# Optimization experiments

Measured on AMD Instinct MI355X. Metric: run time of the kernel, lower is better.

Reference implementation:

```python
import jax, jax.numpy as jnp
import numpy as np

HIDDEN = 2048
NUM_HEADS = 16
NUM_KV_HEADS = 4
HEAD_DIM = HIDDEN // NUM_HEADS  # 128
GROUPS = NUM_HEADS // NUM_KV_HEADS  # 4
ROPE_DIMS = 32
QK_GAIN = 6.0
B, T = 2, 2048


def _rope_cos_sin(T, dtype):
    pos = jnp.arange(T, dtype=jnp.float32)
    inv_freq = 1.0 / (10000.0 ** (jnp.arange(0, ROPE_DIMS, 2, dtype=jnp.float32) / ROPE_DIMS))
    freqs = jnp.outer(pos, inv_freq)                  # [T, ROPE/2]
    freqs = jnp.concatenate([freqs, freqs], axis=-1)  # [T, ROPE]
    return jnp.cos(freqs).astype(dtype), jnp.sin(freqs).astype(dtype)


def _apply_rope(t, cos_f, sin_f):
    # t: [B, H, T, head_dim]; rope on first ROPE_DIMS, pass-through on the rest
    t_rt, t_pass = t[..., :ROPE_DIMS], t[..., ROPE_DIMS:]
    h1, h2 = jnp.split(t_rt, 2, axis=-1)
    rot = jnp.concatenate([-h2, h1], axis=-1)
    return jnp.concatenate([t_rt * cos_f + rot * sin_f, t_pass], axis=-1)


def setup_inputs() -> dict:
    key = jax.random.key(0)
    ks = jax.random.split(key, 5)
    s = 0.02
    return {
        "x": jax.random.normal(ks[0], (B, T, HIDDEN), jnp.float32),
        "Wq": jax.random.normal(ks[1], (HIDDEN, HIDDEN), jnp.float32) * s,
        "Wk": jax.random.normal(ks[2], (HIDDEN, NUM_KV_HEADS * HEAD_DIM), jnp.float32) * s,
        "Wv": jax.random.normal(ks[3], (HIDDEN, NUM_KV_HEADS * HEAD_DIM), jnp.float32) * s,
        "Wo": jax.random.normal(ks[4], (HIDDEN, HIDDEN), jnp.float32) * s,
    }


def reference(x, Wq, Wk, Wv, Wo):
    Bx, Tx, C = x.shape
    q = (x @ Wq).reshape(Bx, Tx, NUM_HEADS, HEAD_DIM).transpose(0, 2, 1, 3)      # [B,H,T,d]
    k = (x @ Wk).reshape(Bx, Tx, NUM_KV_HEADS, HEAD_DIM).transpose(0, 2, 1, 3)   # [B,KV,T,d]
    v = (x @ Wv).reshape(Bx, Tx, NUM_KV_HEADS, HEAD_DIM).transpose(0, 2, 1, 3)   # [B,KV,T,d]

    cos_f, sin_f = _rope_cos_sin(Tx, q.dtype)  # [T, ROPE]
    q = _apply_rope(q, cos_f, sin_f)
    k = _apply_rope(k, cos_f, sin_f)

    # GQA: group query heads per kv head instead of repeat_interleave-ing K/V
    qg = q.reshape(Bx, NUM_KV_HEADS, GROUPS, Tx, HEAD_DIM)
    scale = QK_GAIN / jnp.sqrt(jnp.asarray(HEAD_DIM, q.dtype))
    scores = jnp.einsum('bkgqd,bkld->bkgql', qg * scale, k)  # [B,KV,G,T,T]
    causal = jnp.tril(jnp.ones((Tx, Tx), dtype=bool))
    scores = jnp.where(causal, scores, jnp.asarray(-jnp.inf, scores.dtype))
    probs = jax.nn.softmax(scores, axis=-1)
    out = jnp.einsum('bkgql,bkld->bkgqd', probs, v)          # [B,KV,G,T,d]
    out = out.reshape(Bx, NUM_HEADS, Tx, HEAD_DIM).transpose(0, 2, 1, 3).reshape(Bx, Tx, C)
    return out @ Wo
```

## Files before the change

kernel.cpp:

```cpp
#include <hip/hip_runtime.h>
#include <hip/hip_bf16.h>
#include <cstdint>
#include <cstddef>

typedef unsigned short u16;
typedef short s16x8 __attribute__((ext_vector_type(8)));
typedef float f32x4 __attribute__((ext_vector_type(4)));
typedef float f32x16 __attribute__((ext_vector_type(16)));
typedef u16 u16x4 __attribute__((ext_vector_type(4)));

#define HIDDEN_C 2048
#define TSEQ 2048
#define BATCH 2
#define NHEADS 16
#define NKV 4
#define HDIM 128
#define NQKV 3072
#define BTR 4096
#define QK_SCALE 0.53033008588991f

__device__ __forceinline__ float bf2f(u16 u) {
  union { uint32_t i; float f; } v; v.i = ((uint32_t)u) << 16; return v.f;
}
__device__ __forceinline__ u16 f2bf(float f) {
  union { float f; uint32_t i; } v; v.f = f;
  uint32_t r = v.i + 0x7fffu + ((v.i >> 16) & 1u);
  return (u16)(r >> 16);
}

#define AS1(p) ((__attribute__((address_space(1))) void*)(uintptr_t)(p))
#define AS3(p) ((__attribute__((address_space(3))) void*)(p))

__global__ void convert_x_kernel(const float* __restrict__ x, u16* __restrict__ xb) {
  int i = (blockIdx.x * blockDim.x + threadIdx.x) * 8;
  float4 a = *(const float4*)(x + i);
  float4 b = *(const float4*)(x + i + 4);
  uint4 o;
  o.x = (uint32_t)f2bf(a.x) | ((uint32_t)f2bf(a.y) << 16);
  o.y = (uint32_t)f2bf(a.z) | ((uint32_t)f2bf(a.w) << 16);
  o.z = (uint32_t)f2bf(b.x) | ((uint32_t)f2bf(b.y) << 16);
  o.w = (uint32_t)f2bf(b.z) | ((uint32_t)f2bf(b.w) << 16);
  *(uint4*)(xb + i) = o;
}

__global__ void rope_table_kernel(float2* __restrict__ tab) {
  int idx = blockIdx.x * blockDim.x + threadIdx.x;
  int t = idx >> 4, i = idx & 15;
  float f = powf(10000.f, -(float)i * (1.f / 16.f));
  float ang = (float)t * f;
  tab[idx] = make_float2(cosf(ang), sinf(ang));
}

__global__ void transpose_w_kernel(const float* __restrict__ in, u16* __restrict__ out,
                                   int R, int C) {
  __shared__ float tile[32][33];
  int r0 = blockIdx.y * 32, c0 = blockIdx.x * 32;
  int tx = threadIdx.x, ty = threadIdx.y;
  #pragma unroll
  for (int i = 0; i < 32; i += 8)
    tile[ty + i][tx] = in[(size_t)(r0 + ty + i) * C + c0 + tx];
  __syncthreads();
  #pragma unroll
  for (int i = 0; i < 32; i += 8)
    out[(size_t)(c0 + ty + i) * R + r0 + tx] = f2bf(tile[tx][ty + i]);
}

template <typename OutT>
__global__ __launch_bounds__(256) void gemm_bt_kernel(const u16* __restrict__ A,
                                                      const u16* __restrict__ BT,
                                                      OutT* __restrict__ C,
                                                      int M, int N, int K,
                                                      const float2* __restrict__ tab,
                                                      int mode) {
  __shared__ u16 As[128 * 32];
  __shared__ u16 Bs[128 * 32];
  const int tid = threadIdx.x;
  const int wave = tid >> 6, lane = tid & 63;
  const int lr = lane & 15, lg = lane >> 4;
  const int m0 = blockIdx.y * 128, n0 = blockIdx.x * 128;
  const int wr = wave >> 1, wc = wave & 1;
  f32x4 acc[4][4];
  #pragma unroll
  for (int a = 0; a < 4; ++a)
    #pragma unroll
    for (int b = 0; b < 4; ++b) acc[a][b] = (f32x4){0.f, 0.f, 0.f, 0.f};

  for (int k0 = 0; k0 < K; k0 += 32) {
    #pragma unroll
    for (int i = 0; i < 2; ++i) {
      int c = tid + i * 256;
      int row = c >> 2, col8 = (c & 3) * 8;
      const u16* gA = A + (size_t)(m0 + row) * K + k0 + col8;
      const u16* gB = BT + (size_t)(n0 + row) * K + k0 + col8;
      char* lA = (char*)As + ((size_t)(wave * 64 + i * 256)) * 16;
      char* lB = (char*)Bs + ((size_t)(wave * 64 + i * 256)) * 16;
      __builtin_amdgcn_global_load_lds(AS1(gA), AS3(lA), 16, 0, 0);
      __builtin_amdgcn_global_load_lds(AS1(gB), AS3(lB), 16, 0, 0);
    }
    __syncthreads();
    s16x8 af[4], bfr[4];
    #pragma unroll
    for (int mi = 0; mi < 4; ++mi)
      af[mi] = *(const s16x8*)(As + (wr * 64 + mi * 16 + lr) * 32 + lg * 8);
    #pragma unroll
    for (int ni = 0; ni < 4; ++ni)
      bfr[ni] = *(const s16x8*)(Bs + (wc * 64 + ni * 16 + lr) * 32 + lg * 8);
    #pragma unroll
    for (int mi = 0; mi < 4; ++mi)
      #pragma unroll
      for (int ni = 0; ni < 4; ++ni)
        acc[mi][ni] = __builtin_amdgcn_mfma_f32_16x16x32_bf16(af[mi], bfr[ni], acc[mi][ni], 0, 0, 0);
    __syncthreads();
  }
  if (mode) {
    if (n0 < 2560 && wc == 0) {
      #pragma unroll
      for (int mi = 0; mi < 4; ++mi) {
        int rowb = m0 + wr * 64 + mi * 16 + lg * 4;
        #pragma unroll
        for (int r = 0; r < 4; ++r) {
          int t = (rowb + r) & (TSEQ - 1);
          float2 cs = tab[(t << 4) | lr];
          float a = acc[mi][0][r], b2 = acc[mi][1][r];
          acc[mi][0][r] = a * cs.x - b2 * cs.y;
          acc[mi][1][r] = b2 * cs.x + a * cs.y;
        }
      }
    }
    if (n0 < 2048) {
      #pragma unroll
      for (int mi = 0; mi < 4; ++mi)
        #pragma unroll
        for (int ni = 0; ni < 4; ++ni)
          #pragma unroll
          for (int r = 0; r < 4; ++r) acc[mi][ni][r] *= QK_SCALE;
    }
  }
  #pragma unroll
  for (int mi = 0; mi < 4; ++mi) {
    int rowb = m0 + wr * 64 + mi * 16 + lg * 4;
    #pragma unroll
    for (int ni = 0; ni < 4; ++ni) {
      int col = n0 + wc * 64 + ni * 16 + lr;
      #pragma unroll
      for (int r = 0; r < 4; ++r) {
        float v = acc[mi][ni][r];
        if constexpr (sizeof(OutT) == 2) C[(size_t)(rowb + r) * N + col] = (OutT)f2bf(v);
        else                             C[(size_t)(rowb + r) * N + col] = v;
      }
    }
  }
}

__global__ void transpose_v_kernel(const u16* __restrict__ qkv, u16* __restrict__ vt) {
  int bg = blockIdx.z;
  int b = bg >> 2, g = bg & 3;
  int t0 = blockIdx.x * 32, d0 = blockIdx.y * 32;
  __shared__ u16 tile[32][33];
  int tx = threadIdx.x, ty = threadIdx.y;
  #pragma unroll
  for (int i = 0; i < 32; i += 8)
    tile[ty + i][tx] = qkv[(size_t)(b * TSEQ + t0 + ty + i) * NQKV + 2560 + g * HDIM + d0 + tx];
  __syncthreads();
  #pragma unroll
  for (int i = 0; i < 32; i += 8)
    vt[((size_t)bg * HDIM + d0 + ty + i) * TSEQ + t0 + tx] = tile[tx][ty + i];
}

__global__ __launch_bounds__(256, 2) void attn_kernel(const u16* __restrict__ qkv,
                                                      const u16* __restrict__ vt,
                                                      u16* __restrict__ attn_out) {
  __shared__ u16 K_lds[2][64][128];
  __shared__ u16 V_lds[2][128][64];
  __shared__ u16 P_lds[4][32][64];

  const int idx = blockIdx.x;
  const int h = idx & 15, b = (idx >> 4) & 1, g = h >> 2;
  const int jb = (idx >> 5) & 7;
  const int tile = (idx >> 8) ? jb : 15 - jb;
  const int tid = threadIdx.x, w = tid >> 6, lane = tid & 63;
  const int lq = lane & 31;
  const int hf = lane >> 5;
  const int q0 = tile * 128;
  const int q0w = q0 + w * 32;
  const int swz = (lane & 7) << 3;
  const int pswz = lq & 7;

  const u16* Qg = qkv + (size_t)b * TSEQ * NQKV + h * HDIM;
  const u16* Kg = qkv + (size_t)b * TSEQ * NQKV + HIDDEN_C + g * HDIM;
  const u16* Vg = vt + (size_t)(b * NKV + g) * HDIM * TSEQ;

  s16x8 aq[8];
  {
    const u16* qrow = Qg + (size_t)(q0w + lq) * NQKV + hf * 8;
    #pragma unroll
    for (int ds = 0; ds < 8; ++ds) aq[ds] = *(const s16x8*)(qrow + ds * 16);
  }

  f32x16 O[4];
  #pragma unroll
  for (int dt = 0; dt < 4; ++dt)
    #pragma unroll
    for (int r = 0; r < 16; ++r) O[dt][r] = 0.f;
  float m_r = -1e30f, l_r = 0.f;

  auto STAGE = [&](int buf, int kb) {
    #pragma unroll
    for (int i = 0; i < 4; ++i) {
      int c = tid + i * 256;
      int row = c >> 4, slot = c & 15;
      int gslot = slot ^ (row & 7);
      const u16* src = Kg + (size_t)(kb + row) * NQKV + gslot * 8;
      char* dst = (char*)&K_lds[buf][0][0] + (size_t)c * 16;
      __builtin_amdgcn_global_load_lds(AS1(src), AS3(dst), 16, 0, 0);
    }
    #pragma unroll
    for (int i = 0; i < 4; ++i) {
      int c = tid + i * 256;
      int row = c >> 3, slot = c & 7;
      int gslot = slot ^ (row & 7);
      const u16* src = Vg + (size_t)row * TSEQ + kb + gslot * 8;
      char* dst = (char*)&V_lds[buf][0][0] + (size_t)c * 16;
      __builtin_amdgcn_global_load_lds(AS1(src), AS3(dst), 16, 0, 0);
    }
  };

  const int nt = (q0 + 128) / 64;
  STAGE(0, 0);
  asm volatile("s_waitcnt vmcnt(0)" ::: "memory");
  __syncthreads();

  for (int t = 0; t < nt; ++t) {
    const int kb = t * 64;
    const int cur = t & 1;
    if (t + 1 < nt) STAGE(cur ^ 1, kb + 64);

    if (kb <= q0w + 31) {
      f32x16 S[2];
      #pragma unroll
      for (int kh = 0; kh < 2; ++kh)
        #pragma unroll
        for (int r = 0; r < 16; ++r) S[kh][r] = 0.f;
      __builtin_amdgcn_s_setprio(1);
      #pragma unroll
      for (int kh = 0; kh < 2; ++kh) {
        const u16* krow = &K_lds[cur][kh * 32 + lq][0];
        #pragma unroll
        for (int ds = 0; ds < 8; ++ds) {
          s16x8 ak = *(const s16x8*)(krow + ((ds * 16 + hf * 8) ^ swz));
          S[kh] = __builtin_amdgcn_mfma_f32_32x32x16_bf16(ak, aq[ds], S[kh], 0, 0, 0);
        }
      }
      __builtin_amdgcn_s_setprio(0);
      if (kb + 63 > q0w) {
        const int q = q0w + lq;
        #pragma unroll
        for (int kh = 0; kh < 2; ++kh)
          #pragma unroll
          for (int r = 0; r < 16; ++r) {
            int k = kb + kh * 32 + (r & 3) + 8 * (r >> 2) + 4 * hf;
            if (k > q) S[kh][r] = -1e30f;
          }
      }
      f32x16 pm;
      #pragma unroll
      for (int r = 0; r < 16; ++r) pm[r] = fmaxf(S[0][r], S[1][r]);
      float m8[8];
      #pragma unroll
      for (int r = 0; r < 8; ++r) m8[r] = fmaxf(pm[r], pm[r + 8]);
      float mx = fmaxf(fmaxf(fmaxf(m8[0], m8[4]), fmaxf(m8[1], m8[5])),
                       fmaxf(fmaxf(m8[2], m8[6]), fmaxf(m8[3], m8[7])));
      mx = fmaxf(mx, __shfl_xor(mx, 32));
      const float mn = fmaxf(m_r, mx);
      const float al = __expf(m_r - mn);
      m_r = mn;
      #pragma unroll
      for (int kh = 0; kh < 2; ++kh)
        #pragma unroll
        for (int r = 0; r < 16; ++r) S[kh][r] = __expf(S[kh][r] - mn);
      f32x16 sv;
      #pragma unroll
      for (int r = 0; r < 16; ++r) sv[r] = S[0][r] + S[1][r];
      float s8[8];
      #pragma unroll
      for (int r = 0; r < 8; ++r) s8[r] = sv[r] + sv[r + 8];
      float ps = ((s8[0] + s8[4]) + (s8[1] + s8[5])) + ((s8[2] + s8[6]) + (s8[3] + s8[7]));
      ps += __shfl_xor(ps, 32);
      l_r = l_r * al + ps;
      #pragma unroll
      for (int dt = 0; dt < 4; ++dt)
        #pragma unroll
        for (int r = 0; r < 16; ++r) O[dt][r] *= al;
      u16* pw = &P_lds[w][lq][0];
      #pragma unroll
      for (int kh = 0; kh < 2; ++kh)
        #pragma unroll
        for (int r2 = 0; r2 < 4; ++r2) {
          u16x4 hq;
          #pragma unroll
          for (int j = 0; j < 4; ++j) hq[j] = f2bf(S[kh][r2 * 4 + j]);
          int slot = kh * 4 + r2;
          *(u16x4*)(pw + ((slot ^ pswz) << 3) + hf * 4) = hq;
        }
      asm volatile("s_waitcnt lgkmcnt(0)" ::: "memory");
      __builtin_amdgcn_sched_barrier(0);
      s16x8 pb[4];
      #pragma unroll
      for (int ks = 0; ks < 4; ++ks) {
        int slot = ks * 2 + hf;
        pb[ks] = *(const s16x8*)(pw + ((slot ^ pswz) << 3));
      }
      __builtin_amdgcn_s_setprio(1);
      #pragma unroll
      for (int dt = 0; dt < 4; ++dt) {
        const u16* vrow = &V_lds[cur][dt * 32 + lq][0];
        #pragma unroll
        for (int ks = 0; ks < 4; ++ks) {
          s16x8 av = *(const s16x8*)(vrow + ((ks * 16 + hf * 8) ^ swz));
          O[dt] = __builtin_amdgcn_mfma_f32_32x32x16_bf16(av, pb[ks], O[dt], 0, 0, 0);
        }
      }
      __builtin_amdgcn_s_setprio(0);
    }
    asm volatile("s_waitcnt vmcnt(0)" ::: "memory");
    __syncthreads();
  }

  const float invl = 1.f / l_r;
  u16* orow = attn_out + (size_t)(b * TSEQ + q0w + lq) * HIDDEN_C + h * HDIM + hf * 4;
  #pragma unroll
  for (int dt = 0; dt < 4; ++dt)
    #pragma unroll
    for (int r2 = 0; r2 < 4; ++r2) {
      u16x4 o4;
      #pragma unroll
      for (int j = 0; j < 4; ++j) o4[j] = f2bf(O[dt][r2 * 4 + j] * invl);
      *(u16x4*)(orow + dt * 32 + r2 * 8) = o4;
    }
}

extern "C" void kernel_launch(void* const* d_in, const int* in_sizes, int n_in,
                              void* d_out, int out_size, void* d_ws, size_t ws_size,
                              hipStream_t stream) {
  const float* x  = (const float*)d_in[0];
  const float* Wq = (const float*)d_in[1];
  const float* Wk = (const float*)d_in[2];
  const float* Wv = (const float*)d_in[3];
  const float* Wo = (const float*)d_in[4];
  float* out = (float*)d_out;
  char* ws = (char*)d_ws;

  u16* xb    = (u16*)(ws);
  u16* wqkvT = (u16*)(ws + (size_t)(16u << 20));
  u16* woT   = (u16*)(ws + (size_t)(28u << 20));
  u16* qkv   = (u16*)(ws + (size_t)(36u << 20));
  u16* vtb   = (u16*)(ws + (size_t)(60u << 20));
  u16* attn  = (u16*)(ws + (size_t)(64u << 20));
  float2* rope_tab = (float2*)(ws + (size_t)(64u << 20));

  dim3 tb(32, 8);
  convert_x_kernel<<<(BTR * HIDDEN_C / 8) / 256, 256, 0, stream>>>(x, xb);
  rope_table_kernel<<<(TSEQ * 16) / 256, 256, 0, stream>>>(rope_tab);
  transpose_w_kernel<<<dim3(HIDDEN_C / 32, HIDDEN_C / 32), tb, 0, stream>>>(Wq, wqkvT, HIDDEN_C, HIDDEN_C);
  transpose_w_kernel<<<dim3(512 / 32, HIDDEN_C / 32), tb, 0, stream>>>(Wk, wqkvT + (size_t)2048 * 2048, HIDDEN_C, 512);
  transpose_w_kernel<<<dim3(512 / 32, HIDDEN_C / 32), tb, 0, stream>>>(Wv, wqkvT + (size_t)2560 * 2048, HIDDEN_C, 512);
  transpose_w_kernel<<<dim3(HIDDEN_C / 32, HIDDEN_C / 32), tb, 0, stream>>>(Wo, woT, HIDDEN_C, HIDDEN_C);

  gemm_bt_kernel<u16><<<dim3(NQKV / 128, BTR / 128), 256, 0, stream>>>(
      xb, wqkvT, qkv, BTR, NQKV, HIDDEN_C, rope_tab, 1);

  transpose_v_kernel<<<dim3(TSEQ / 32, HDIM / 32, BATCH * NKV), tb, 0, stream>>>(qkv, vtb);

  attn_kernel<<<512, 256, 0, stream>>>(qkv, vtb, attn);

  gemm_bt_kernel<float><<<dim3(HIDDEN_C / 128, BTR / 128), 256, 0, stream>>>(
      attn, woT, out, BTR, HIDDEN_C, HIDDEN_C, nullptr, 0);
}
```

Measured before the change: 234.9 us.

## Double GEMM K-tile with XOR-swizzled LDS and merge prep kernels

The GEMM now stages 64-wide K tiles instead of 32 and uses an XOR swizzle on the LDS slot index to avoid bank conflicts on fragment reads. This halves the number of barriers per K loop, at the cost of twice the LDS per block. Separately, the rope table build is folded into the x-conversion kernel, and the four weight-transpose launches become one 3D launch, which cuts launch overhead. Blocks in the merged transpose grid that fall outside the narrower K/V weights exit early.

```diff
diff --git a/kernel.cpp b/kernel.cpp
--- a/kernel.cpp
+++ b/kernel.cpp
@@ -31,8 +31,16 @@
 #define AS1(p) ((__attribute__((address_space(1))) void*)(uintptr_t)(p))
 #define AS3(p) ((__attribute__((address_space(3))) void*)(p))
 
-__global__ void convert_x_kernel(const float* __restrict__ x, u16* __restrict__ xb) {
-  int i = (blockIdx.x * blockDim.x + threadIdx.x) * 8;
+__global__ void convert_x_kernel(const float* __restrict__ x, u16* __restrict__ xb,
+                                 float2* __restrict__ tab) {
+  int gi = blockIdx.x * blockDim.x + threadIdx.x;
+  if (gi < TSEQ * 16) {
+    int t = gi >> 4, i = gi & 15;
+    float f = powf(10000.f, -(float)i * (1.f / 16.f));
+    float ang = (float)t * f;
+    tab[gi] = make_float2(cosf(ang), sinf(ang));
+  }
+  int i = gi * 8;
   float4 a = *(const float4*)(x + i);
   float4 b = *(const float4*)(x + i + 4);
   uint4 o;
@@ -43,18 +51,23 @@
   *(uint4*)(xb + i) = o;
 }
 
-__global__ void rope_table_kernel(float2* __restrict__ tab) {
-  int idx = blockIdx.x * blockDim.x + threadIdx.x;
-  int t = idx >> 4, i = idx & 15;
-  float f = powf(10000.f, -(float)i * (1.f / 16.f));
-  float ang = (float)t * f;
-  tab[idx] = make_float2(cosf(ang), sinf(ang));
-}
-
-__global__ void transpose_w_kernel(const float* __restrict__ in, u16* __restrict__ out,
-                                   int R, int C) {
+__global__ void transpose_w_kernel(const float* __restrict__ Wq,
+                                   const float* __restrict__ Wk,
+                                   const float* __restrict__ Wv,
+                                   const float* __restrict__ Wo,
+                                   u16* __restrict__ wqkvT,
+                                   u16* __restrict__ woT) {
+  const int z = blockIdx.z;
+  const float* in; u16* out; int C;
+  switch (z) {
+    case 0: in = Wq; out = wqkvT;                        C = 2048; break;
+    case 1: in = Wk; out = wqkvT + (size_t)2048 * 2048;  C = 512;  break;
+    case 2: in = Wv; out = wqkvT + (size_t)2560 * 2048;  C = 512;  break;
+    default: in = Wo; out = woT;                         C = 2048; break;
+  }
+  int r0 = blockIdx.y * 32, c0 = blockIdx.x * 32;
+  if (c0 >= C) return;
   __shared__ float tile[32][33];
-  int r0 = blockIdx.y * 32, c0 = blockIdx.x * 32;
   int tx = threadIdx.x, ty = threadIdx.y;
   #pragma unroll
   for (int i = 0; i < 32; i += 8)
@@ -62,7 +75,7 @@
   __syncthreads();
   #pragma unroll
   for (int i = 0; i < 32; i += 8)
-    out[(size_t)(c0 + ty + i) * R + r0 + tx] = f2bf(tile[tx][ty + i]);
+    out[(size_t)(c0 + ty + i) * 2048 + r0 + tx] = f2bf(tile[tx][ty + i]);
 }
 
 template <typename OutT>
@@ -72,44 +85,49 @@
                                                       int M, int N, int K,
                                                       const float2* __restrict__ tab,
                                                       int mode) {
-  __shared__ u16 As[128 * 32];
-  __shared__ u16 Bs[128 * 32];
+  __shared__ u16 As[128 * 64];
+  __shared__ u16 Bs[128 * 64];
   const int tid = threadIdx.x;
   const int wave = tid >> 6, lane = tid & 63;
   const int lr = lane & 15, lg = lane >> 4;
   const int m0 = blockIdx.y * 128, n0 = blockIdx.x * 128;
   const int wr = wave >> 1, wc = wave & 1;
+  const int fsw = (lr & 7) << 3;
   f32x4 acc[4][4];
   #pragma unroll
   for (int a = 0; a < 4; ++a)
     #pragma unroll
     for (int b = 0; b < 4; ++b) acc[a][b] = (f32x4){0.f, 0.f, 0.f, 0.f};
 
-  for (int k0 = 0; k0 < K; k0 += 32) {
-    #pragma unroll
-    for (int i = 0; i < 2; ++i) {
+  for (int k0 = 0; k0 < K; k0 += 64) {
+    #pragma unroll
+    for (int i = 0; i < 4; ++i) {
       int c = tid + i * 256;
-      int row = c >> 2, col8 = (c & 3) * 8;
-      const u16* gA = A + (size_t)(m0 + row) * K + k0 + col8;
-      const u16* gB = BT + (size_t)(n0 + row) * K + k0 + col8;
-      char* lA = (char*)As + ((size_t)(wave * 64 + i * 256)) * 16;
-      char* lB = (char*)Bs + ((size_t)(wave * 64 + i * 256)) * 16;
+      int row = c >> 3, slot = c & 7;
+      int gslot = slot ^ (row & 7);
+      const u16* gA = A + (size_t)(m0 + row) * K + k0 + gslot * 8;
+      const u16* gB = BT + (size_t)(n0 + row) * K + k0 + gslot * 8;
+      char* lA = (char*)As + (size_t)c * 16;
+      char* lB = (char*)Bs + (size_t)c * 16;
       __builtin_amdgcn_global_load_lds(AS1(gA), AS3(lA), 16, 0, 0);
       __builtin_amdgcn_global_load_lds(AS1(gB), AS3(lB), 16, 0, 0);
     }
     __syncthreads();
-    s16x8 af[4], bfr[4];
-    #pragma unroll
-    for (int mi = 0; mi < 4; ++mi)
-      af[mi] = *(const s16x8*)(As + (wr * 64 + mi * 16 + lr) * 32 + lg * 8);
-    #pragma unroll
-    for (int ni = 0; ni < 4; ++ni)
-      bfr[ni] = *(const s16x8*)(Bs + (wc * 64 + ni * 16 + lr) * 32 + lg * 8);
-    #pragma unroll
-    for (int mi = 0; mi < 4; ++mi)
+    #pragma unroll
+    for (int kk = 0; kk < 2; ++kk) {
+      s16x8 af[4], bfr[4];
+      #pragma unroll
+      for (int mi = 0; mi < 4; ++mi)
+        af[mi] = *(const s16x8*)(As + (wr * 64 + mi * 16 + lr) * 64 + ((kk * 32 + lg * 8) ^ fsw));
       #pragma unroll
       for (int ni = 0; ni < 4; ++ni)
-        acc[mi][ni] = __builtin_amdgcn_mfma_f32_16x16x32_bf16(af[mi], bfr[ni], acc[mi][ni], 0, 0, 0);
+        bfr[ni] = *(const s16x8*)(Bs + (wc * 64 + ni * 16 + lr) * 64 + ((kk * 32 + lg * 8) ^ fsw));
+      #pragma unroll
+      for (int mi = 0; mi < 4; ++mi)
+        #pragma unroll
+        for (int ni = 0; ni < 4; ++ni)
+          acc[mi][ni] = __builtin_amdgcn_mfma_f32_16x16x32_bf16(af[mi], bfr[ni], acc[mi][ni], 0, 0, 0);
+    }
     __syncthreads();
   }
   if (mode) {
@@ -359,12 +377,8 @@
   float2* rope_tab = (float2*)(ws + (size_t)(64u << 20));
 
   dim3 tb(32, 8);
-  convert_x_kernel<<<(BTR * HIDDEN_C / 8) / 256, 256, 0, stream>>>(x, xb);
-  rope_table_kernel<<<(TSEQ * 16) / 256, 256, 0, stream>>>(rope_tab);
-  transpose_w_kernel<<<dim3(HIDDEN_C / 32, HIDDEN_C / 32), tb, 0, stream>>>(Wq, wqkvT, HIDDEN_C, HIDDEN_C);
-  transpose_w_kernel<<<dim3(512 / 32, HIDDEN_C / 32), tb, 0, stream>>>(Wk, wqkvT + (size_t)2048 * 2048, HIDDEN_C, 512);
-  transpose_w_kernel<<<dim3(512 / 32, HIDDEN_C / 32), tb, 0, stream>>>(Wv, wqkvT + (size_t)2560 * 2048, HIDDEN_C, 512);
-  transpose_w_kernel<<<dim3(HIDDEN_C / 32, HIDDEN_C / 32), tb, 0, stream>>>(Wo, woT, HIDDEN_C, HIDDEN_C);
+  convert_x_kernel<<<(BTR * HIDDEN_C / 8) / 256, 256, 0, stream>>>(x, xb, rope_tab);
+  transpose_w_kernel<<<dim3(64, 64, 4), tb, 0, stream>>>(Wq, Wk, Wv, Wo, wqkvT, woT);
 
   gemm_bt_kernel<u16><<<dim3(NQKV / 128, BTR / 128), 256, 0, stream>>>(
       xb, wqkvT, qkv, BTR, NQKV, HIDDEN_C, rope_tab, 1);
```

After: 210.8 us. 1.11x faster.
